# Optimization experiments

Hardware: AMD Instinct MI355X
Metric: run time of the kernel (lower is better)

Reference implementation:

```python
import jax, jax.numpy as jnp
import numpy as np

B, C, H, W = 4, 512, 32, 32
HEADS = 8
EPS = 1e-5


def setup_inputs() -> dict:
    key = jax.random.key(0)
    ks = jax.random.split(key, 9)
    s = 1.0 / np.sqrt(C)
    return {
        "x": jax.random.normal(ks[0], (B, C, H, W), dtype=jnp.float32),
        "w_q": jax.random.normal(ks[1], (C, C), dtype=jnp.float32) * s,  # Conv2d 1x1, no bias
        "w_k": jax.random.normal(ks[2], (C, C), dtype=jnp.float32) * s,
        "w_v": jax.random.normal(ks[3], (C, C), dtype=jnp.float32) * s,
        "w_head": jax.random.normal(ks[4], (HEADS, HEADS), dtype=jnp.float32) * (1.0 / np.sqrt(HEADS)),
        "in_gamma": jnp.ones((HEADS,), dtype=jnp.float32) + 0.1 * jax.random.normal(ks[5], (HEADS,), dtype=jnp.float32),
        "in_beta": 0.1 * jax.random.normal(ks[6], (HEADS,), dtype=jnp.float32),
        "w_proj": jax.random.normal(ks[7], (C, C), dtype=jnp.float32) * s,
        "b_proj": 0.02 * jax.random.normal(ks[8], (C,), dtype=jnp.float32),
    }


def reference(x, w_q, w_k, w_v, w_head, in_gamma, in_beta, w_proj, b_proj):
    b, c, h, w = x.shape
    heads = w_head.shape[0]
    hd = c // heads
    t = h * w
    scale = hd ** (-0.5)

    xf = x.reshape(b, c, t)  # [B,C,T]
    # 1x1 convs == channel matmuls
    q = jnp.einsum('oc,bct->bot', w_q, xf).reshape(b, heads, hd, t)
    k = jnp.einsum('oc,bct->bot', w_k, xf).reshape(b, heads, hd, t)
    v = jnp.einsum('oc,bct->bot', w_v, xf).reshape(b, heads, hd, t)

    attn = jnp.einsum('bhdq,bhdT->bhqT', q, k) * scale           # [B,heads,T,T]
    attn = jnp.einsum('gh,bhqT->bgqT', w_head, attn)             # head-mixing 1x1 conv
    attn = jax.nn.softmax(attn, axis=-1)
    # InstanceNorm2d over the (T,T) spatial dims, per head, biased variance
    mean = jnp.mean(attn, axis=(-2, -1), keepdims=True)
    var = jnp.var(attn, axis=(-2, -1), keepdims=True)
    attn = (attn - mean) / jnp.sqrt(var + EPS)
    attn = attn * in_gamma[None, :, None, None] + in_beta[None, :, None, None]

    out = jnp.einsum('bhqT,bhdT->bhqd', attn, v)                 # [B,heads,T,hd]
    out = out.reshape(b, t, c)                                   # same row-major flatten as torch .view
    out = out @ w_proj.T + b_proj                                # Linear
    return out.transpose(0, 2, 1).reshape(b, c, h, w)
```

## Files before the change

kernel.cpp:

```cpp
#include <hip/hip_runtime.h>
#include <hip/hip_bf16.h>

#define B_ 4
#define C_ 512
#define T_ 1024
#define SCALE_ 0.125f
#define EPS_ 1e-5f

typedef unsigned short u16;
typedef __attribute__((ext_vector_type(8))) unsigned short u16x8;
typedef __attribute__((ext_vector_type(4))) unsigned short u16x4;
typedef __attribute__((ext_vector_type(8))) short s16x8;
typedef __attribute__((ext_vector_type(4))) float f32x4;

#define QT_OFF    (0x0ull)
#define KS_OFF    (0x400000ull)
#define VS_OFF    (0x800000ull)
#define XT_OFF    (0xC00000ull)
#define O_OFF     (0x1000000ull)
#define LSUM_OFF  (0x1440000ull)
#define L2SUM_OFF (0x1460000ull)
#define WB_OFF    (0x1480000ull)
#define LP_OFF    (0x1680000ull)
#define L2P_OFF   (0x1700000ull)
#define WS_OFF    (0x1780000ull)
#define VSUM_OFF  (0x17A0000ull)
#define OP_OFF    (0x2000000ull)

static __device__ __forceinline__ u16 f2bf(float f) {
  unsigned u = __float_as_uint(f);
  unsigned r = (u + 0x7fff + ((u >> 16) & 1)) >> 16;
  return (u16)r;
}
static __device__ __forceinline__ float b2f(u16 x) {
  return __uint_as_float(((unsigned)x) << 16);
}
static __device__ __forceinline__ f32x4 mfma16(s16x8 a, s16x8 b, f32x4 c) {
  return __builtin_amdgcn_mfma_f32_16x16x32_bf16(a, b, c, 0, 0, 0);
}

__global__ __launch_bounds__(256) void prep_k(
    const float* __restrict__ x, const float* __restrict__ wq,
    const float* __restrict__ wk, const float* __restrict__ wv,
    const float* __restrict__ wp, u16* __restrict__ wb,
    float* __restrict__ ws, float* __restrict__ vsum, u16* __restrict__ xt) {
  const int id = blockIdx.x;
  const int tid = threadIdx.x;
  __shared__ float Ts[64][65];
  if (id < 512) {
    const int i = (id << 8) + tid;
    const int idx = i << 3;
    const int which = idx >> 18;
    const int off = idx & 262143;
    const float* s = which == 0 ? wq : which == 1 ? wk : which == 2 ? wv : wp;
    const float4 f0 = *(const float4*)(s + off);
    const float4 f1 = *(const float4*)(s + off + 4);
    u16x8 o;
    o[0] = f2bf(f0.x); o[1] = f2bf(f0.y); o[2] = f2bf(f0.z); o[3] = f2bf(f0.w);
    o[4] = f2bf(f1.x); o[5] = f2bf(f1.y); o[6] = f2bf(f1.z); o[7] = f2bf(f1.w);
    *(u16x8*)(wb + idx) = o;
  } else if (id < 640) {
    const int idx = ((id - 512) << 8) + tid;
    if (id - 512 < 8) vsum[idx] = 0.f;
    const int o = idx >> 6, d = idx & 63;
    float s = 0.f;
#pragma unroll
    for (int j = 0; j < 8; ++j) s += wp[(o << 9) + (j << 6) + d];
    ws[idx] = s;
  } else {
    const int id3 = id - 640;
    const int b = id3 >> 7, rem = id3 & 127;
    const int t0 = (rem & 15) << 6;
    const int c0 = (rem >> 4) << 6;
    const float* __restrict__ X = x + (size_t)b * (C_ * (size_t)T_);
    u16* __restrict__ Xt = xt + (size_t)b * (T_ * (size_t)C_);
#pragma unroll
    for (int i = 0; i < 4; ++i) {
      const int e = tid + (i << 8);
      const int r = e >> 4, c4 = e & 15;
      const float4 v =
          *(const float4*)(X + (size_t)(c0 + r) * T_ + t0 + (c4 << 2));
      Ts[r][(c4 << 2) + 0] = v.x; Ts[r][(c4 << 2) + 1] = v.y;
      Ts[r][(c4 << 2) + 2] = v.z; Ts[r][(c4 << 2) + 3] = v.w;
    }
    __syncthreads();
#pragma unroll
    for (int i = 0; i < 2; ++i) {
      const int e = tid + (i << 8);
      const int tt = e >> 3, c8 = e & 7;
      u16x8 o;
#pragma unroll
      for (int j = 0; j < 8; ++j) o[j] = f2bf(Ts[(c8 << 3) + j][tt]);
      *(u16x8*)(Xt + (size_t)(t0 + tt) * C_ + c0 + (c8 << 3)) = o;
    }
  }
}

__global__ __launch_bounds__(256) void gemm_qkv(
    const u16* __restrict__ xt, const u16* __restrict__ wqb,
    const u16* __restrict__ wkb, const u16* __restrict__ wvb,
    u16* __restrict__ qto, u16* __restrict__ ks, u16* __restrict__ vs,
    float* __restrict__ vsum) {
  const int z = blockIdx.z;
  const int tid = threadIdx.x;
  const int w = tid >> 6, lane = tid & 63, lr = lane & 15, lq = lane >> 4;
  const int wm = (w >> 1) << 6, wn = (w & 1) << 5;
  __shared__ __align__(16) u16 As[128][72];
  __shared__ __align__(16) u16 Bs[64][72];
  u16* Ts = &As[0][0];
  const u16 *Ag, *Bg;
  int m0, n0, mode, b;
  if (z < 8) {
    const int which = z >> 2;
    b = z & 3;
    Ag = xt + (size_t)b * (T_ * (size_t)C_);
    m0 = blockIdx.x << 7;
    Bg = which ? wkb : wqb;
    n0 = blockIdx.y << 6;
    mode = which;
  } else {
    b = z - 8;
    const int ti = (blockIdx.y << 3) | blockIdx.x;
    Ag = wvb;
    m0 = (ti >> 4) << 7;
    Bg = xt + (size_t)b * (T_ * (size_t)C_);
    n0 = (ti & 15) << 6;
    mode = 2;
  }
  f32x4 acc[4][2] = {};
  for (int k0 = 0; k0 < C_; k0 += 64) {
#pragma unroll
    for (int it = 0; it < 4; ++it) {
      const int e = tid + (it << 8);
      const int r = e >> 3, c8 = (e & 7) << 3;
      *(u16x8*)&As[r][c8] =
          *(const u16x8*)(Ag + (size_t)(m0 + r) * C_ + k0 + c8);
    }
#pragma unroll
    for (int it = 0; it < 2; ++it) {
      const int e = tid + (it << 8);
      const int r = e >> 3, c8 = (e & 7) << 3;
      *(u16x8*)&Bs[r][c8] =
          *(const u16x8*)(Bg + (size_t)(n0 + r) * C_ + k0 + c8);
    }
    __syncthreads();
#pragma unroll
    for (int kf = 0; kf < 2; ++kf) {
      const int ko = (kf << 5) + (lq << 3);
      s16x8 a[4], bb[2];
#pragma unroll
      for (int i = 0; i < 4; ++i) a[i] = *(const s16x8*)&As[wm + (i << 4) + lr][ko];
#pragma unroll
      for (int j = 0; j < 2; ++j) bb[j] = *(const s16x8*)&Bs[wn + (j << 4) + lr][ko];
#pragma unroll
      for (int i = 0; i < 4; ++i)
#pragma unroll
        for (int j = 0; j < 2; ++j) acc[i][j] = mfma16(a[i], bb[j], acc[i][j]);
    }
    __syncthreads();
  }
  if (mode == 0) {
    u16* Y = qto + (size_t)b * (T_ * (size_t)C_);
#pragma unroll
    for (int i = 0; i < 4; ++i) {
      const int row = wm + (i << 4) + (lq << 2);
#pragma unroll
      for (int j = 0; j < 2; ++j) {
        const int col = wn + (j << 4) + lr;
#pragma unroll
        for (int r = 0; r < 4; ++r)
          Y[(size_t)(m0 + row + r) * C_ + n0 + col] =
              f2bf(acc[i][j][r] * SCALE_);
      }
    }
    return;
  }
  if (mode == 2) {
#pragma unroll
    for (int i = 0; i < 4; ++i)
#pragma unroll
      for (int r = 0; r < 4; ++r) {
        float s = acc[i][0][r] + acc[i][1][r];
        s += __shfl_xor(s, 1, 64);
        s += __shfl_xor(s, 2, 64);
        s += __shfl_xor(s, 4, 64);
        s += __shfl_xor(s, 8, 64);
        if (lr == 0) {
          const int o = m0 + wm + (i << 4) + (lq << 2) + r;
          atomicAdd(&vsum[(((b << 3) | (o >> 6)) << 6) | (o & 63)], s);
        }
      }
  }
#pragma unroll
  for (int i = 0; i < 4; ++i)
#pragma unroll
    for (int j = 0; j < 2; ++j)
#pragma unroll
      for (int r = 0; r < 4; ++r)
        Ts[(wm + (i << 4) + (lq << 2) + r) * 72 + wn + (j << 4) + lr] =
            f2bf(acc[i][j][r]);
  __syncthreads();
  const int ch = tid >> 4, part = tid & 15;
  if (mode == 1) {
    const int t32l = ch >> 2, half = (ch >> 1) & 1, fl = ch & 1;
    const int t32g = (m0 >> 5) + t32l, fg = (n0 >> 5) + fl;
    u16* dst =
        ks + (((((size_t)((b << 5) | t32g) << 1) | half) << 4 | fg) << 9);
#pragma unroll
    for (int u = 0; u < 4; ++u) {
      const int lanek = (u << 4) + part;
      const int quadk = lanek >> 4, lrk = lanek & 15;
      const int rr = ((lrk >> 2) << 3) | (half << 2) | (lrk & 3);
      const u16x8 v =
          *(const u16x8*)&Ts[((t32l << 5) + rr) * 72 + (fl << 5) + (quadk << 3)];
      *(u16x8*)(dst + (lanek << 3)) = v;
    }
  } else {
    const int gl = ch >> 3, t32l = (ch >> 2) & 1, dj = ch & 3;
    const int gg = (m0 >> 6) + gl, t32g = (n0 >> 5) + t32l;
    u16* dst =
        vs + (((((size_t)((b << 3) | gg) << 5) | t32g) << 2 | dj) << 9);
#pragma unroll
    for (int u = 0; u < 4; ++u) {
      const int lanev = (u << 4) + part;
      const int quadv = lanev >> 4, lrv = lanev & 15;
      const u16x8 v = *(const u16x8*)&Ts[((gl << 6) + (dj << 4) + lrv) * 72 +
                                         (t32l << 5) + (quadv << 3)];
      *(u16x8*)(dst + (lanev << 3)) = v;
    }
  }
}

__global__ __launch_bounds__(512, 4) void attn_fused(
    const u16* __restrict__ Qt, const u16* __restrict__ KS,
    const u16* __restrict__ VS, const float* __restrict__ wh,
    float* __restrict__ Opart, float* __restrict__ lpart,
    float* __restrict__ l2part) {
  const int id = blockIdx.x;
  const int xcd = id & 7;
  const int b = xcd >> 1;
  const int hi = id >> 3;
  const int qb = ((xcd & 1) << 5) | (hi & 31);
  const int tq = hi >> 5;
  const int q0 = qb << 4;
  const int tid = threadIdx.x;
  const int w = tid >> 6, lane = tid & 63;
  const int lr = lane & 15, quad = lane >> 4;

  __shared__ __align__(16) u16 Qs[16][522];
  __shared__ __align__(16) u16 Plds[8][16][136];
  float* Sbuf = (float*)&Plds[0][0][0];

  {
    const u16* Qb = Qt + ((size_t)b * T_ + q0) * C_;
    for (int i = tid; i < 1024; i += 512) {
      const int r = i >> 6, c8 = i & 63;
      *(u16x8*)&Qs[r][c8 << 3] = *(const u16x8*)(Qb + (size_t)r * C_ + (c8 << 3));
    }
  }

  const u16* __restrict__ Qrow = &Qs[lr][quad << 3];
  const int g = w;
  const int win = w >> 1, half = w & 1;
  const int swz = lr & 7;
  const u16* __restrict__ Vc =
      VS + (((size_t)((b << 3) | g)) << 16) + (lane << 3);

  float lacc[8] = {}, l2acc[8] = {};
  f32x4 acc[4] = {};

  __syncthreads();

  for (int c = 0; c < 4; ++c) {
    const int t32k = (tq << 4) + (c << 2) + win;
    const u16* __restrict__ Kc =
        KS + (((size_t)((((b << 5) | t32k) << 1) | half)) << 13) + (lane << 3);
    f32x4 m[8] = {};
#pragma unroll 4
    for (int h = 0; h < 8; ++h) {
      f32x4 a0 = {0.f, 0.f, 0.f, 0.f};
      const s16x8 qf0 = *(const s16x8*)(Qrow + (h << 6));
      const s16x8 k0 = *(const s16x8*)(Kc + (h << 10));
      a0 = mfma16(k0, qf0, a0);
      const s16x8 qf1 = *(const s16x8*)(Qrow + (h << 6) + 32);
      const s16x8 k1 = *(const s16x8*)(Kc + (h << 10) + 512);
      a0 = mfma16(k1, qf1, a0);
#pragma unroll
      for (int gg = 0; gg < 8; ++gg) {
        const float wgh = wh[(gg << 3) + h];
        m[gg] += a0 * wgh;
      }
    }
    const int wgrp = ((win << 2) | quad) ^ swz;
#pragma unroll
    for (int gg = 0; gg < 8; ++gg) {
      f32x4 e0;
#pragma unroll
      for (int k = 0; k < 4; ++k) e0[k] = __expf(m[gg][k]);
      u16x4 o;
#pragma unroll
      for (int k = 0; k < 4; ++k) o[k] = f2bf(e0[k]);
      *(u16x4*)&Plds[gg][lr][(wgrp << 3) + (half << 2)] = o;
      lacc[gg] += e0[0] + e0[1] + e0[2] + e0[3];
      l2acc[gg] += e0[0] * e0[0] + e0[1] * e0[1] + e0[2] * e0[2] + e0[3] * e0[3];
    }
    __syncthreads();
#pragma unroll
    for (int tw = 0; tw < 4; ++tw) {
      const int t32v = (tq << 4) + (c << 2) + tw;
      const int rgrp = ((tw << 2) | quad) ^ swz;
      const s16x8 pa = *(const s16x8*)&Plds[g][lr][rgrp << 3];
#pragma unroll
      for (int dj = 0; dj < 4; ++dj) {
        const s16x8 vb =
            *(const s16x8*)(Vc + ((size_t)t32v << 11) + (dj << 9));
        acc[dj] = mfma16(pa, vb, acc[dj]);
      }
    }
    __syncthreads();
  }

  const int bg = (b << 3) + g;
  const size_t obase = ((((size_t)(tq << 5) + bg) << 10) + q0) * 64;
#pragma unroll
  for (int dj = 0; dj < 4; ++dj) {
    const int d = (dj << 4) + lr;
#pragma unroll
    for (int r = 0; r < 4; ++r) {
      const int q = (quad << 2) + r;
      Opart[obase + (size_t)q * 64 + d] = acc[dj][r];
    }
  }

  float* lbuf = Sbuf;
  float* l2buf = Sbuf + 1024;
#pragma unroll
  for (int gg = 0; gg < 8; ++gg) {
    float l = lacc[gg];
    l += __shfl_xor(l, 16, 64);
    l += __shfl_xor(l, 32, 64);
    float l2 = l2acc[gg];
    l2 += __shfl_xor(l2, 16, 64);
    l2 += __shfl_xor(l2, 32, 64);
    if (quad == 0) {
      lbuf[(w << 7) + (gg << 4) + lr] = l;
      l2buf[(w << 7) + (gg << 4) + lr] = l2;
    }
  }
  __syncthreads();
  if (lane < 16) {
    float l = 0.f, l2 = 0.f;
#pragma unroll
    for (int w2 = 0; w2 < 8; ++w2) {
      l += lbuf[(w2 << 7) + (g << 4) + lr];
      l2 += l2buf[(w2 << 7) + (g << 4) + lr];
    }
    const size_t li = (((size_t)(tq << 5) + bg) << 10) + q0 + lr;
    lpart[li] = l;
    l2part[li] = l2;
  }
}

__global__ __launch_bounds__(256) void combine_o(
    const float* __restrict__ Opart, const float* __restrict__ lpart,
    const float* __restrict__ l2part, u16* __restrict__ O,
    float* __restrict__ lsum, float* __restrict__ l2sum) {
  const int bg = blockIdx.x;
  const int qo = blockIdx.y;
  const int tid = threadIdx.x;
  const int q = (qo << 7) + (tid >> 1);
  const int d0 = (tid & 1) << 5;
  float l = 0.f, l2 = 0.f;
#pragma unroll
  for (int tq = 0; tq < 2; ++tq) {
    const size_t li = (((size_t)(tq << 5) + bg) << 10) + q;
    l += lpart[li];
    l2 += l2part[li];
  }
  const float linv = 1.f / l;
  if ((tid & 1) == 0) {
    lsum[((size_t)bg << 10) + q] = l;
    l2sum[((size_t)bg << 10) + q] = l2;
  }
  f32x4 a[8] = {};
#pragma unroll
  for (int tq = 0; tq < 2; ++tq) {
    const float* src =
        Opart + ((((size_t)(tq << 5) + bg) << 10) + q) * 64 + d0;
#pragma unroll
    for (int j = 0; j < 8; ++j) a[j] += *(const f32x4*)(src + (j << 2));
  }
  u16* dst = O + (((size_t)bg << 10) + q) * 64 + d0;
#pragma unroll
  for (int j = 0; j < 4; ++j) {
    u16x8 o;
#pragma unroll
    for (int k = 0; k < 4; ++k) {
      o[k] = f2bf(a[2 * j][k] * linv);
      o[k + 4] = f2bf(a[2 * j + 1][k] * linv);
    }
    *(u16x8*)(dst + (j << 3)) = o;
  }
}

__global__ __launch_bounds__(256) void gemm_proj(
    const u16* __restrict__ O, const u16* __restrict__ wpb,
    const float* __restrict__ lsum, const float* __restrict__ l2sum,
    const float* __restrict__ gamma, const float* __restrict__ beta,
    const float* __restrict__ ws, const float* __restrict__ bp,
    const float* __restrict__ vsum, float* __restrict__ y) {
  const int b = blockIdx.z;
  const int m0 = blockIdx.y << 6;
  const int n0 = blockIdx.x << 6;
  const int gidx = blockIdx.x >> 1;
  const int bg = (b << 3) + gidx;
  const u16* __restrict__ Ob = O + (size_t)b * (8 * T_ * 64);
  __shared__ u16 As[64][72];
  __shared__ u16 Bs[64][72];
  __shared__ float red[4];
  __shared__ float albc[2];
  __shared__ float b2s[64];
  const int tid = threadIdx.x;
  const int w = tid >> 6, lane = tid & 63, lr = lane & 15, lq = lane >> 4;
  const int mw = (w >> 1) << 5, nw = (w & 1) << 5;
  {
    const f32x4 l = *(const f32x4*)(lsum + ((size_t)bg << 10) + (tid << 2));
    const f32x4 l2 = *(const f32x4*)(l2sum + ((size_t)bg << 10) + (tid << 2));
    float ssq = 0.f;
#pragma unroll
    for (int k = 0; k < 4; ++k) ssq += l2[k] / (l[k] * l[k]);
#pragma unroll
    for (int off = 32; off; off >>= 1) ssq += __shfl_xor(ssq, off, 64);
    if (lane == 0) red[w] = ssq;
  }
  __syncthreads();
  if (tid == 0) {
    const float s = red[0] + red[1] + red[2] + red[3];
    const float mean = 0.0009765625f;
    const float var = s * (1.f / 1048576.f) - mean * mean;
    const float al = gamma[gidx] * rsqrtf(var + EPS_);
    albc[0] = al;
    albc[1] = beta[gidx] - al * mean;
  }
  __syncthreads();
  if (tid < 64) {
    const int o = m0 + tid;
    const float* wr = ws + (o << 6);
    const float* vsr = vsum + (bg << 6);
    float acc = 0.f;
#pragma unroll
    for (int d = 0; d < 64; d += 4) {
      const float4 vv4 = *(const float4*)(vsr + d);
      const float4 ws4 = *(const float4*)(wr + d);
      acc += ws4.x * vv4.x + ws4.y * vv4.y + ws4.z * vv4.z + ws4.w * vv4.w;
    }
    b2s[tid] = bp[o] + albc[1] * acc;
  }
  f32x4 acc[2][2] = {};
  for (int k0 = 0; k0 < C_; k0 += 64) {
    if (k0 == 0) __syncthreads();
#pragma unroll
    for (int it = 0; it < 2; ++it) {
      const int e = tid + (it << 8);
      const int r = e >> 3, c8 = e & 7;
      *(u16x8*)&As[r][c8 << 3] =
          *(const u16x8*)(wpb + (size_t)(m0 + r) * C_ + k0 + (c8 << 3));
      const int t = n0 + r;
      const int c = k0 + (c8 << 3);
      *(u16x8*)&Bs[r][c8 << 3] =
          *(const u16x8*)(Ob + (size_t)(t >> 7) * (T_ * 64) +
                          (size_t)(((t & 127) << 3) + (c >> 6)) * 64 + (c & 63));
    }
    __syncthreads();
#pragma unroll
    for (int kf = 0; kf < 2; ++kf) {
      const int ko = (kf << 5) + (lq << 3);
      s16x8 a[2], bb[2];
#pragma unroll
      for (int i = 0; i < 2; ++i) a[i] = *(const s16x8*)&As[mw + (i << 4) + lr][ko];
#pragma unroll
      for (int j = 0; j < 2; ++j) bb[j] = *(const s16x8*)&Bs[nw + (j << 4) + lr][ko];
#pragma unroll
      for (int i = 0; i < 2; ++i)
#pragma unroll
        for (int j = 0; j < 2; ++j) acc[i][j] = mfma16(a[i], bb[j], acc[i][j]);
    }
    __syncthreads();
  }
  const float al = albc[0];
#pragma unroll
  for (int i = 0; i < 2; ++i) {
    const int row = mw + (i << 4) + (lq << 2);
#pragma unroll
    for (int j = 0; j < 2; ++j) {
      const int col = nw + (j << 4) + lr;
#pragma unroll
      for (int r = 0; r < 4; ++r)
        y[(size_t)b * (C_ * (size_t)T_) + (size_t)(m0 + row + r) * T_ + n0 + col] =
            acc[i][j][r] * al + b2s[row + r];
    }
  }
}

extern "C" void kernel_launch(void* const* d_in, const int* in_sizes, int n_in,
                              void* d_out, int out_size, void* d_ws,
                              size_t ws_size, hipStream_t stream) {
  const float* x = (const float*)d_in[0];
  const float* wq = (const float*)d_in[1];
  const float* wk = (const float*)d_in[2];
  const float* wv = (const float*)d_in[3];
  const float* wh = (const float*)d_in[4];
  const float* gm = (const float*)d_in[5];
  const float* bt = (const float*)d_in[6];
  const float* wp = (const float*)d_in[7];
  const float* bp = (const float*)d_in[8];
  float* y = (float*)d_out;
  char* wsb = (char*)d_ws;

  u16* Qt = (u16*)(wsb + QT_OFF);
  u16* KS = (u16*)(wsb + KS_OFF);
  u16* VS = (u16*)(wsb + VS_OFF);
  u16* Xt = (u16*)(wsb + XT_OFF);
  u16* Og = (u16*)(wsb + O_OFF);
  float* vsum = (float*)(wsb + VSUM_OFF);
  float* lsum = (float*)(wsb + LSUM_OFF);
  float* l2sum = (float*)(wsb + L2SUM_OFF);
  u16* Wb = (u16*)(wsb + WB_OFF);
  u16* WQb = Wb;
  u16* WKb = Wb + 262144;
  u16* WVb = Wb + 524288;
  u16* WPb = Wb + 786432;
  float* lpart = (float*)(wsb + LP_OFF);
  float* l2part = (float*)(wsb + L2P_OFF);
  float* ws = (float*)(wsb + WS_OFF);
  float* Opart = (float*)(wsb + OP_OFF);

  prep_k<<<dim3(1152), 256, 0, stream>>>(x, wq, wk, wv, wp, Wb, ws, vsum, Xt);
  gemm_qkv<<<dim3(8, 8, 12), 256, 0, stream>>>(Xt, WQb, WKb, WVb, Qt, KS, VS,
                                               vsum);
  attn_fused<<<dim3(512), 512, 0, stream>>>(Qt, KS, VS, wh, Opart, lpart,
                                            l2part);
  combine_o<<<dim3(32, 8), 256, 0, stream>>>(Opart, lpart, l2part, Og, lsum,
                                             l2sum);
  gemm_proj<<<dim3(16, 8, 4), 256, 0, stream>>>(Og, WPb, lsum, l2sum, gm, bt,
                                                ws, bp, vsum, y);
}
```

Measured before the change: 158.6 us.

## Fuse split-partial combine into projection GEMM and prefetch GEMM tiles into registers

Removes the combine_o kernel. gemm_proj now reads the fp32 attention partials and row sums directly, sums the two splits and applies the 1/l normalisation while staging the B tile into shared memory. Both the QKV and projection GEMMs gain register double-buffering: the next K tile is loaded into registers while the current one is computed, with lighter barriers. This saves a launch and the intermediate bf16 O round trip, but each projection block now rereads larger fp32 partial data.

```diff
diff --git a/kernel.cpp b/kernel.cpp
--- a/kernel.cpp
+++ b/kernel.cpp
@@ -17,9 +17,6 @@
 #define KS_OFF    (0x400000ull)
 #define VS_OFF    (0x800000ull)
 #define XT_OFF    (0xC00000ull)
-#define O_OFF     (0x1000000ull)
-#define LSUM_OFF  (0x1440000ull)
-#define L2SUM_OFF (0x1460000ull)
 #define WB_OFF    (0x1480000ull)
 #define LP_OFF    (0x1680000ull)
 #define L2P_OFF   (0x1700000ull)
@@ -38,6 +35,11 @@
 static __device__ __forceinline__ f32x4 mfma16(s16x8 a, s16x8 b, f32x4 c) {
   return __builtin_amdgcn_mfma_f32_16x16x32_bf16(a, b, c, 0, 0, 0);
 }
+#define BARSYNC()                                       \
+  {                                                     \
+    asm volatile("s_waitcnt lgkmcnt(0)" ::: "memory");  \
+    __builtin_amdgcn_s_barrier();                       \
+  }
 
 __global__ __launch_bounds__(256) void prep_k(
     const float* __restrict__ x, const float* __restrict__ wq,
@@ -127,23 +129,36 @@
     n0 = (ti & 15) << 6;
     mode = 2;
   }
+  u16x8 rA[4], rB[2];
+#define LOADQ(K)                                                          \
+  {                                                                       \
+    _Pragma("unroll") for (int it = 0; it < 4; ++it) {                    \
+      const int e = tid + (it << 8);                                      \
+      const int r = e >> 3, c8 = (e & 7) << 3;                            \
+      rA[it] = *(const u16x8*)(Ag + (size_t)(m0 + r) * C_ + (K) + c8);    \
+    }                                                                     \
+    _Pragma("unroll") for (int it = 0; it < 2; ++it) {                    \
+      const int e = tid + (it << 8);                                      \
+      const int r = e >> 3, c8 = (e & 7) << 3;                            \
+      rB[it] = *(const u16x8*)(Bg + (size_t)(n0 + r) * C_ + (K) + c8);    \
+    }                                                                     \
+  }
   f32x4 acc[4][2] = {};
+  LOADQ(0);
   for (int k0 = 0; k0 < C_; k0 += 64) {
+    if (k0) BARSYNC();
 #pragma unroll
     for (int it = 0; it < 4; ++it) {
       const int e = tid + (it << 8);
-      const int r = e >> 3, c8 = (e & 7) << 3;
-      *(u16x8*)&As[r][c8] =
-          *(const u16x8*)(Ag + (size_t)(m0 + r) * C_ + k0 + c8);
+      *(u16x8*)&As[e >> 3][(e & 7) << 3] = rA[it];
     }
 #pragma unroll
     for (int it = 0; it < 2; ++it) {
       const int e = tid + (it << 8);
-      const int r = e >> 3, c8 = (e & 7) << 3;
-      *(u16x8*)&Bs[r][c8] =
-          *(const u16x8*)(Bg + (size_t)(n0 + r) * C_ + k0 + c8);
-    }
-    __syncthreads();
+      *(u16x8*)&Bs[e >> 3][(e & 7) << 3] = rB[it];
+    }
+    if (k0 < C_ - 64) LOADQ(k0 + 64);
+    BARSYNC();
 #pragma unroll
     for (int kf = 0; kf < 2; ++kf) {
       const int ko = (kf << 5) + (lq << 3);
@@ -157,8 +172,8 @@
 #pragma unroll
         for (int j = 0; j < 2; ++j) acc[i][j] = mfma16(a[i], bb[j], acc[i][j]);
     }
-    __syncthreads();
-  }
+  }
+#undef LOADQ
   if (mode == 0) {
     u16* Y = qto + (size_t)b * (T_ * (size_t)C_);
 #pragma unroll
@@ -191,6 +206,7 @@
         }
       }
   }
+  BARSYNC();
 #pragma unroll
   for (int i = 0; i < 4; ++i)
 #pragma unroll
@@ -361,51 +377,9 @@
   }
 }
 
-__global__ __launch_bounds__(256) void combine_o(
-    const float* __restrict__ Opart, const float* __restrict__ lpart,
-    const float* __restrict__ l2part, u16* __restrict__ O,
-    float* __restrict__ lsum, float* __restrict__ l2sum) {
-  const int bg = blockIdx.x;
-  const int qo = blockIdx.y;
-  const int tid = threadIdx.x;
-  const int q = (qo << 7) + (tid >> 1);
-  const int d0 = (tid & 1) << 5;
-  float l = 0.f, l2 = 0.f;
-#pragma unroll
-  for (int tq = 0; tq < 2; ++tq) {
-    const size_t li = (((size_t)(tq << 5) + bg) << 10) + q;
-    l += lpart[li];
-    l2 += l2part[li];
-  }
-  const float linv = 1.f / l;
-  if ((tid & 1) == 0) {
-    lsum[((size_t)bg << 10) + q] = l;
-    l2sum[((size_t)bg << 10) + q] = l2;
-  }
-  f32x4 a[8] = {};
-#pragma unroll
-  for (int tq = 0; tq < 2; ++tq) {
-    const float* src =
-        Opart + ((((size_t)(tq << 5) + bg) << 10) + q) * 64 + d0;
-#pragma unroll
-    for (int j = 0; j < 8; ++j) a[j] += *(const f32x4*)(src + (j << 2));
-  }
-  u16* dst = O + (((size_t)bg << 10) + q) * 64 + d0;
-#pragma unroll
-  for (int j = 0; j < 4; ++j) {
-    u16x8 o;
-#pragma unroll
-    for (int k = 0; k < 4; ++k) {
-      o[k] = f2bf(a[2 * j][k] * linv);
-      o[k + 4] = f2bf(a[2 * j + 1][k] * linv);
-    }
-    *(u16x8*)(dst + (j << 3)) = o;
-  }
-}
-
 __global__ __launch_bounds__(256) void gemm_proj(
-    const u16* __restrict__ O, const u16* __restrict__ wpb,
-    const float* __restrict__ lsum, const float* __restrict__ l2sum,
+    const float* __restrict__ Opart, const u16* __restrict__ wpb,
+    const float* __restrict__ lpart, const float* __restrict__ l2part,
     const float* __restrict__ gamma, const float* __restrict__ beta,
     const float* __restrict__ ws, const float* __restrict__ bp,
     const float* __restrict__ vsum, float* __restrict__ y) {
@@ -414,24 +388,55 @@
   const int n0 = blockIdx.x << 6;
   const int gidx = blockIdx.x >> 1;
   const int bg = (b << 3) + gidx;
-  const u16* __restrict__ Ob = O + (size_t)b * (8 * T_ * 64);
-  __shared__ u16 As[64][72];
-  __shared__ u16 Bs[64][72];
+  __shared__ __align__(16) u16 As[64][72];
+  __shared__ __align__(16) u16 Bs[64][72];
   __shared__ float red[4];
   __shared__ float albc[2];
   __shared__ float b2s[64];
+  __shared__ float linvS[512];
   const int tid = threadIdx.x;
   const int w = tid >> 6, lane = tid & 63, lr = lane & 15, lq = lane >> 4;
   const int mw = (w >> 1) << 5, nw = (w & 1) << 5;
+  u16x8 rA[2];
+  f32x4 rB[2][2][2];
+#define LOADP(K)                                                            \
+  {                                                                         \
+    _Pragma("unroll") for (int it = 0; it < 2; ++it) {                      \
+      const int e = tid + (it << 8);                                        \
+      const int r = e >> 3, c8 = (e & 7) << 3;                              \
+      rA[it] = *(const u16x8*)(wpb + (size_t)(m0 + r) * C_ + (K) + c8);     \
+      const int q = (((n0 + r) & 127) << 3) + ((K) >> 6);                   \
+      _Pragma("unroll") for (int tq = 0; tq < 2; ++tq) {                    \
+        const float* src =                                                  \
+            Opart + ((((size_t)((tq << 5) + bg)) << 10) + q) * 64 + c8;     \
+        rB[it][tq][0] = *(const f32x4*)(src);                               \
+        rB[it][tq][1] = *(const f32x4*)(src + 4);                           \
+      }                                                                     \
+    }                                                                       \
+  }
+  LOADP(0);
   {
-    const f32x4 l = *(const f32x4*)(lsum + ((size_t)bg << 10) + (tid << 2));
-    const f32x4 l2 = *(const f32x4*)(l2sum + ((size_t)bg << 10) + (tid << 2));
+    const size_t p0 = ((size_t)bg) << 10, p1 = ((size_t)(32 + bg)) << 10;
+    const f32x4 la = *(const f32x4*)(lpart + p0 + (tid << 2));
+    const f32x4 lb = *(const f32x4*)(lpart + p1 + (tid << 2));
+    const f32x4 l2a = *(const f32x4*)(l2part + p0 + (tid << 2));
+    const f32x4 l2b = *(const f32x4*)(l2part + p1 + (tid << 2));
     float ssq = 0.f;
 #pragma unroll
-    for (int k = 0; k < 4; ++k) ssq += l2[k] / (l[k] * l[k]);
+    for (int k = 0; k < 4; ++k) {
+      const float l = la[k] + lb[k];
+      ssq += (l2a[k] + l2b[k]) / (l * l);
+    }
 #pragma unroll
     for (int off = 32; off; off >>= 1) ssq += __shfl_xor(ssq, off, 64);
     if (lane == 0) red[w] = ssq;
+    const int qb0 = (n0 & 127) << 3;
+#pragma unroll
+    for (int j = 0; j < 2; ++j) {
+      const int qq = (tid << 1) + j;
+      const float l = lpart[p0 + qb0 + qq] + lpart[p1 + qb0 + qq];
+      linvS[qq] = 1.f / l;
+    }
   }
   __syncthreads();
   if (tid == 0) {
@@ -458,20 +463,24 @@
   }
   f32x4 acc[2][2] = {};
   for (int k0 = 0; k0 < C_; k0 += 64) {
-    if (k0 == 0) __syncthreads();
+    if (k0) BARSYNC();
+    __syncthreads();
 #pragma unroll
     for (int it = 0; it < 2; ++it) {
       const int e = tid + (it << 8);
-      const int r = e >> 3, c8 = e & 7;
-      *(u16x8*)&As[r][c8 << 3] =
-          *(const u16x8*)(wpb + (size_t)(m0 + r) * C_ + k0 + (c8 << 3));
-      const int t = n0 + r;
-      const int c = k0 + (c8 << 3);
-      *(u16x8*)&Bs[r][c8 << 3] =
-          *(const u16x8*)(Ob + (size_t)(t >> 7) * (T_ * 64) +
-                          (size_t)(((t & 127) << 3) + (c >> 6)) * 64 + (c & 63));
-    }
-    __syncthreads();
+      const int r = e >> 3, c8 = (e & 7) << 3;
+      *(u16x8*)&As[r][c8] = rA[it];
+      const float li = linvS[(r << 3) + (k0 >> 6)];
+      u16x8 o;
+#pragma unroll
+      for (int k = 0; k < 4; ++k) {
+        o[k] = f2bf((rB[it][0][0][k] + rB[it][1][0][k]) * li);
+        o[k + 4] = f2bf((rB[it][0][1][k] + rB[it][1][1][k]) * li);
+      }
+      *(u16x8*)&Bs[r][c8] = o;
+    }
+    if (k0 < C_ - 64) LOADP(k0 + 64);
+    BARSYNC();
 #pragma unroll
     for (int kf = 0; kf < 2; ++kf) {
       const int ko = (kf << 5) + (lq << 3);
@@ -485,8 +494,8 @@
 #pragma unroll
         for (int j = 0; j < 2; ++j) acc[i][j] = mfma16(a[i], bb[j], acc[i][j]);
     }
-    __syncthreads();
-  }
+  }
+#undef LOADP
   const float al = albc[0];
 #pragma unroll
   for (int i = 0; i < 2; ++i) {
@@ -521,10 +530,7 @@
   u16* KS = (u16*)(wsb + KS_OFF);
   u16* VS = (u16*)(wsb + VS_OFF);
   u16* Xt = (u16*)(wsb + XT_OFF);
-  u16* Og = (u16*)(wsb + O_OFF);
   float* vsum = (float*)(wsb + VSUM_OFF);
-  float* lsum = (float*)(wsb + LSUM_OFF);
-  float* l2sum = (float*)(wsb + L2SUM_OFF);
   u16* Wb = (u16*)(wsb + WB_OFF);
   u16* WQb = Wb;
   u16* WKb = Wb + 262144;
@@ -540,8 +546,6 @@
                                                vsum);
   attn_fused<<<dim3(512), 512, 0, stream>>>(Qt, KS, VS, wh, Opart, lpart,
                                             l2part);
-  combine_o<<<dim3(32, 8), 256, 0, stream>>>(Opart, lpart, l2part, Og, lsum,
-                                             l2sum);
-  gemm_proj<<<dim3(16, 8, 4), 256, 0, stream>>>(Og, WPb, lsum, l2sum, gm, bt,
-                                                ws, bp, vsum, y);
-}
+  gemm_proj<<<dim3(16, 8, 4), 256, 0, stream>>>(Opart, WPb, lpart, l2part, gm,
+                                                bt, ws, bp, vsum, y);
+}
```

After: 150.1 us. -5.3%, faster.
